# Kernel optimization log

Measured on AMD Instinct MI355X. Metric: run time of the kernel, lower is better.

The kernel has to match this reference:

```python
import jax, jax.numpy as jnp
import numpy as np

B, N, FEAT, HID, HEADS = 16, 1024, 512, 1024, 2

def setup_inputs() -> dict:
    key = jax.random.key(0)
    ks = jax.random.split(key, 20)
    s = 0.03
    d = {
        'Fs':  jax.random.normal(ks[0], (B, N, FEAT), jnp.float32),
        'Fq':  jax.random.normal(ks[1], (B, N, FEAT), jnp.float32),
        'Fms': jax.random.normal(ks[2], (B, N, FEAT), jnp.float32),
        'out_dim': N,
        'W1': jax.random.normal(ks[3], (FEAT, FEAT), jnp.float32) * s,
        'W2': jax.random.normal(ks[4], (FEAT, FEAT), jnp.float32) * s,
        'W3': jax.random.normal(ks[5], (FEAT, FEAT), jnp.float32) * s,
        'W4': jax.random.normal(ks[6], (FEAT, FEAT), jnp.float32) * s,
        'W5': jax.random.normal(ks[7], (FEAT, FEAT), jnp.float32) * s,
        'W6': jax.random.normal(ks[8], (FEAT, FEAT), jnp.float32) * s,
        'Wq': jax.random.normal(ks[9], (N, N), jnp.float32) * s,
        'Wk': jax.random.normal(ks[10], (N, N), jnp.float32) * s,
        'Wv': jax.random.normal(ks[11], (N, N), jnp.float32) * s,
        'ln_g': jnp.ones((N,), jnp.float32),
        'ln_b': jnp.zeros((N,), jnp.float32),
        'ffn_w1': jax.random.normal(ks[12], (N, HID), jnp.float32) * s,
        'ffn_w2': jax.random.normal(ks[13], (HID, N), jnp.float32) * s,
        'ffn_ln_g': jnp.ones((N,), jnp.float32),
        'ffn_ln_b': jnp.zeros((N,), jnp.float32),
    }
    return d

def _layernorm(x, g, b, eps):
    mu = x.mean(-1, keepdims=True)
    var = x.var(-1, keepdims=True)
    return (x - mu) * jax.lax.rsqrt(var + eps) * g + b

def _affinity(a, b, Wa, Wb, cl):
    # softmax((a Wa)(b Wb)^T / sqrt(cl)) over last axis
    s = jnp.einsum('bnc,bmc->bnm', a @ Wa, b @ Wb) / jnp.sqrt(jnp.float32(cl))
    return jax.nn.softmax(s, axis=-1)

def reference(Fs, Fq, Fms, out_dim, W1, W2, W3, W4, W5, W6, Wq, Wk, Wv,
              ln_g, ln_b, ffn_w1, ffn_w2, ffn_ln_g, ffn_ln_b):
    ass = _affinity(Fms, Fms, W1, W2, Fms.shape[2])   # [B,N,N]
    asq = _affinity(Fs, Fq, W3, W4, Fs.shape[2])      # [B,N,N]
    aqq = _affinity(Fq, Fq, W5, W6, Fq.shape[2])      # [B,N,N]

    Q, K, V = asq @ Wq, ass @ Wk, asq @ Wv            # [B,N,C], C=N
    Bb, Nn, C = Q.shape
    g = C // HEADS
    def heads(x):
        return x.reshape(Bb, Nn, HEADS, g).transpose(0, 2, 1, 3)  # [B,h,N,g]
    Qs, Ks, Vs = heads(Q), heads(K), heads(V)
    attn = jax.nn.softmax(jnp.einsum('bhqg,bhkg->bhqk', Qs, Ks) / jnp.sqrt(jnp.float32(g)), axis=-1)
    o = jnp.einsum('bhqk,bhkg->bhqg', attn, Vs)
    o = o.transpose(0, 2, 1, 3).reshape(Bb, Nn, C)

    x = _layernorm(o + aqq, ln_g, ln_b, 1e-5)
    y = jnp.maximum(x @ ffn_w1, 0.0) @ ffn_w2 + x     # dropout = identity (eval)
    y = _layernorm(y, ffn_ln_g, ffn_ln_b, 1e-6)
    return y
```

## Files before the change

kernel.cpp:

```cpp
#include <hip/hip_runtime.h>
#include <cstdint>

static constexpr long long Bb = 16, Nn = 1024, FE = 512;
static constexpr long long BN = Bb * Nn;
static constexpr long long E1e = BN * FE;
static constexpr long long E2n = BN * Nn;

static constexpr long long O_WT  = 0;
static constexpr long long SZ_W512 = FE * FE * 2;
static constexpr long long O_WQT = O_WT + 6 * SZ_W512;
static constexpr long long SZ_W1K = Nn * Nn * 2;
static constexpr long long O_WKT = O_WQT + SZ_W1K;
static constexpr long long O_WVT = O_WKT + SZ_W1K;
static constexpr long long O_F1T = O_WVT + SZ_W1K;
static constexpr long long O_F2T = O_F1T + SZ_W1K;
static constexpr long long O_SLOTS = O_F2T + SZ_W1K;
static constexpr long long SLOT = E2n * 2;
static constexpr long long O_S0 = O_SLOTS;
static constexpr long long O_S1 = O_S0 + SLOT;
static constexpr long long O_S2 = O_S1 + SLOT;
static constexpr long long O_E0 = O_S2 + SLOT;
static constexpr long long O_E1 = O_E0 + SLOT;
static constexpr long long O_E2 = O_E1 + SLOT;
static constexpr long long WS_NEED = O_E2 + SLOT;
static constexpr long long O_FMSB = O_E1;
static constexpr long long O_FSB  = O_E1 + E1e * 2;
static constexpr long long O_FQB  = O_E2;
static constexpr long long O_C2   = O_E2 + E1e * 2;

typedef __attribute__((ext_vector_type(8))) short short8;
typedef __attribute__((ext_vector_type(4))) float f32x4;

static __device__ __forceinline__ unsigned short f2bf(float f) {
  union { float f; unsigned u; } x; x.f = f;
  unsigned r = x.u + 0x7FFFu + ((x.u >> 16) & 1u);
  return (unsigned short)(r >> 16);
}
static __device__ __forceinline__ float bf2f(unsigned short h) {
  union { unsigned u; float f; } x; x.u = ((unsigned)h) << 16; return x.f;
}
static __device__ __forceinline__ void gload16(const void* g, void* l) {
  __builtin_amdgcn_global_load_lds(
      (const __attribute__((address_space(1))) unsigned int*)g,
      (__attribute__((address_space(3))) unsigned int*)l, 16, 0, 0);
}

template <int EP>
__global__ __launch_bounds__(256) void gemm_nt(
    const unsigned short* __restrict__ A, long long sA, long long hA, int lda,
    const unsigned short* __restrict__ B, long long sB, long long hB, int ldb,
    void* __restrict__ Cv, long long sC, long long hC, int ldc,
    const void* __restrict__ Rv, long long sR, int K) {
  __shared__ unsigned short lA[128 * 64];
  __shared__ unsigned short lB[64 * 64];
  const int tid = threadIdx.x;
  const int wave = tid >> 6, lane = tid & 63;
  const int wm = wave >> 1, wn = wave & 1;
  const int lrow = lane & 15, quad = lane >> 4;
  const int z = blockIdx.z, z1 = z & 15, z2 = z >> 4;
  const int gy = gridDim.y;
  const int bid = blockIdx.x + gridDim.x * blockIdx.y;
  const int chunk = 8 * gy;
  const int bx = (bid / chunk) * 8 + (bid % 8);
  const int by = (bid % chunk) / 8;
  const long long bm = (long long)bx * 128;
  const long long bn = (long long)by * 64;
  const unsigned short* Ab = A + z1 * sA + z2 * hA + bm * lda;
  const unsigned short* Bbp = B + z1 * sB + z2 * hB + bn * ldb;
  const int srow = lane >> 2;
  const int skol = (lane & 3) * 8;
  const int g0 = wave * 2, g1 = wave * 2 + 1;

  f32x4 acc[4][2];
#pragma unroll
  for (int i = 0; i < 4; ++i)
#pragma unroll
    for (int j = 0; j < 2; ++j) acc[i][j] = (f32x4){0.f, 0.f, 0.f, 0.f};

  for (int k0 = 0; k0 < K; k0 += 64) {
    const unsigned short* Ak = Ab + k0 + skol;
    const unsigned short* Bk = Bbp + k0 + skol;
    gload16(Ak + (long long)(g0 * 16 + srow) * lda,      &lA[g0 * 512 + lane * 8]);
    gload16(Ak + (long long)(g1 * 16 + srow) * lda,      &lA[g1 * 512 + lane * 8]);
    gload16(Ak + (long long)(g0 * 16 + srow) * lda + 32, &lA[4096 + g0 * 512 + lane * 8]);
    gload16(Ak + (long long)(g1 * 16 + srow) * lda + 32, &lA[4096 + g1 * 512 + lane * 8]);
    gload16(Bk + (long long)(wave * 16 + srow) * ldb,      &lB[wave * 512 + lane * 8]);
    gload16(Bk + (long long)(wave * 16 + srow) * ldb + 32, &lB[2048 + wave * 512 + lane * 8]);
    __syncthreads();
#pragma unroll
    for (int p = 0; p < 2; ++p) {
      short8 af[4], bfr[2];
#pragma unroll
      for (int t = 0; t < 4; ++t)
        af[t] = *(const short8*)&lA[p * 4096 + (wm * 64 + t * 16 + lrow) * 32 + quad * 8];
#pragma unroll
      for (int u = 0; u < 2; ++u)
        bfr[u] = *(const short8*)&lB[p * 2048 + (wn * 32 + u * 16 + lrow) * 32 + quad * 8];
#pragma unroll
      for (int mt = 0; mt < 4; ++mt)
#pragma unroll
        for (int nt = 0; nt < 2; ++nt)
          acc[mt][nt] = __builtin_amdgcn_mfma_f32_16x16x32_bf16(af[mt], bfr[nt], acc[mt][nt], 0, 0, 0);
    }
    __syncthreads();
  }
  const long long cm = bm + wm * 64, cn = bn + wn * 32;
  const long long cz = z1 * sC + z2 * hC;
#pragma unroll
  for (int mt = 0; mt < 4; ++mt) {
#pragma unroll
    for (int nt = 0; nt < 2; ++nt) {
      long long col = cn + nt * 16 + lrow;
      long long row0 = cm + mt * 16 + quad * 4;
#pragma unroll
      for (int r = 0; r < 4; ++r) {
        long long row = row0 + r;
        float v = acc[mt][nt][r];
        long long idx = cz + row * ldc + col;
        if (EP == 1) ((unsigned short*)Cv)[idx] = f2bf(v);
        else if (EP == 2) ((unsigned short*)Cv)[idx] = f2bf(v > 0.f ? v : 0.f);
        else {
          float rr = bf2f(((const unsigned short*)Rv)[z1 * sR + row * ldc + col]);
          ((float*)Cv)[idx] = v + rr;
        }
      }
    }
  }
}

__global__ __launch_bounds__(256) void cast3_k(const float* __restrict__ i0,
                                               const float* __restrict__ i1,
                                               const float* __restrict__ i2,
                                               unsigned short* o0, unsigned short* o1,
                                               unsigned short* o2) {
  const float* in = (blockIdx.y == 0) ? i0 : (blockIdx.y == 1) ? i1 : i2;
  unsigned short* out = (blockIdx.y == 0) ? o0 : (blockIdx.y == 1) ? o1 : o2;
  long long i = (long long)blockIdx.x * 256 + threadIdx.x;
  float4 v = ((const float4*)in)[i];
  ushort4 o; o.x = f2bf(v.x); o.y = f2bf(v.y); o.z = f2bf(v.z); o.w = f2bf(v.w);
  ((ushort4*)out)[i] = o;
}

__global__ __launch_bounds__(256) void tcast6_k(const float* p0, const float* p1,
                                                const float* p2, const float* p3,
                                                const float* p4, const float* p5,
                                                unsigned short* outb, int rows, int cols) {
  const float* src[6] = {p0, p1, p2, p3, p4, p5};
  const float* in = src[blockIdx.z];
  unsigned short* out = outb + (long long)blockIdx.z * rows * cols;
  __shared__ float t[32][33];
  const int c0 = blockIdx.x * 32, r0 = blockIdx.y * 32;
  const int tx = threadIdx.x, ty = threadIdx.y;
#pragma unroll
  for (int i = 0; i < 4; ++i) {
    int r = r0 + ty + i * 8;
    t[ty + i * 8][tx] = in[(long long)r * cols + c0 + tx];
  }
  __syncthreads();
#pragma unroll
  for (int i = 0; i < 4; ++i) {
    int c = c0 + ty + i * 8;
    out[(long long)c * rows + r0 + tx] = f2bf(t[tx][ty + i * 8]);
  }
}

__global__ __launch_bounds__(256) void softmax_bf(unsigned short* __restrict__ S, float scale) {
  __shared__ float redA[4], redB[4];
  const long long row = blockIdx.x;
  const int t = threadIdx.x, wave = t >> 6, lane = t & 63;
  ushort4 u = ((ushort4*)(S + row * 1024))[t];
  float v0 = bf2f(u.x) * scale, v1 = bf2f(u.y) * scale, v2 = bf2f(u.z) * scale, v3 = bf2f(u.w) * scale;
  float m = fmaxf(fmaxf(v0, v1), fmaxf(v2, v3));
#pragma unroll
  for (int o = 32; o; o >>= 1) m = fmaxf(m, __shfl_down(m, o));
  if (lane == 0) redA[wave] = m;
  __syncthreads();
  m = fmaxf(fmaxf(redA[0], redA[1]), fmaxf(redA[2], redA[3]));
  float e0 = __expf(v0 - m), e1 = __expf(v1 - m), e2 = __expf(v2 - m), e3 = __expf(v3 - m);
  float s = e0 + e1 + e2 + e3;
#pragma unroll
  for (int o = 32; o; o >>= 1) s += __shfl_down(s, o);
  if (lane == 0) redB[wave] = s;
  __syncthreads();
  s = redB[0] + redB[1] + redB[2] + redB[3];
  float inv = 1.f / s;
  ushort4 ob; ob.x = f2bf(e0 * inv); ob.y = f2bf(e1 * inv); ob.z = f2bf(e2 * inv); ob.w = f2bf(e3 * inv);
  ((ushort4*)(S + row * 1024))[t] = ob;
}

__global__ __launch_bounds__(256) void ln1_k(const unsigned short* __restrict__ O,
                                             const unsigned short* __restrict__ Aq,
                                             const float* __restrict__ g, const float* __restrict__ b,
                                             unsigned short* __restrict__ xb) {
  __shared__ float redA[4], redB[4];
  const long long row = blockIdx.x;
  const int t = threadIdx.x, wave = t >> 6, lane = t & 63;
  ushort4 ou = ((const ushort4*)(O + row * 1024))[t];
  ushort4 au = ((const ushort4*)(Aq + row * 1024))[t];
  float v0 = bf2f(ou.x) + bf2f(au.x), v1 = bf2f(ou.y) + bf2f(au.y);
  float v2 = bf2f(ou.z) + bf2f(au.z), v3 = bf2f(ou.w) + bf2f(au.w);
  float s = v0 + v1 + v2 + v3;
  float q = v0 * v0 + v1 * v1 + v2 * v2 + v3 * v3;
#pragma unroll
  for (int o = 32; o; o >>= 1) { s += __shfl_down(s, o); q += __shfl_down(q, o); }
  if (lane == 0) { redA[wave] = s; redB[wave] = q; }
  __syncthreads();
  float S = redA[0] + redA[1] + redA[2] + redA[3];
  float Q = redB[0] + redB[1] + redB[2] + redB[3];
  float mu = S * (1.f / 1024.f);
  float var = Q * (1.f / 1024.f) - mu * mu;
  float rs = rsqrtf(var + 1e-5f);
  float4 gg = ((const float4*)g)[t], bbv = ((const float4*)b)[t];
  ushort4 ob;
  ob.x = f2bf((v0 - mu) * rs * gg.x + bbv.x);
  ob.y = f2bf((v1 - mu) * rs * gg.y + bbv.y);
  ob.z = f2bf((v2 - mu) * rs * gg.z + bbv.z);
  ob.w = f2bf((v3 - mu) * rs * gg.w + bbv.w);
  ((ushort4*)(xb + row * 1024))[t] = ob;
}

__global__ __launch_bounds__(256) void ln2_k(const float* __restrict__ Y,
                                             const float* __restrict__ g, const float* __restrict__ b,
                                             float* __restrict__ out, float eps) {
  __shared__ float redA[4], redB[4];
  const long long row = blockIdx.x;
  const int t = threadIdx.x, wave = t >> 6, lane = t & 63;
  float4 v = ((const float4*)(Y + row * 1024))[t];
  float s = v.x + v.y + v.z + v.w;
  float q = v.x * v.x + v.y * v.y + v.z * v.z + v.w * v.w;
#pragma unroll
  for (int o = 32; o; o >>= 1) { s += __shfl_down(s, o); q += __shfl_down(q, o); }
  if (lane == 0) { redA[wave] = s; redB[wave] = q; }
  __syncthreads();
  float S = redA[0] + redA[1] + redA[2] + redA[3];
  float Q = redB[0] + redB[1] + redB[2] + redB[3];
  float mu = S * (1.f / 1024.f);
  float var = Q * (1.f / 1024.f) - mu * mu;
  float rs = rsqrtf(var + eps);
  float4 gg = ((const float4*)g)[t], bbv = ((const float4*)b)[t];
  float4 o;
  o.x = (v.x - mu) * rs * gg.x + bbv.x;
  o.y = (v.y - mu) * rs * gg.y + bbv.y;
  o.z = (v.z - mu) * rs * gg.z + bbv.z;
  o.w = (v.w - mu) * rs * gg.w + bbv.w;
  ((float4*)(out + row * 1024))[t] = o;
}

extern "C" void kernel_launch(void* const* d_in, const int* in_sizes, int n_in,
                              void* d_out, int out_size, void* d_ws, size_t ws_size,
                              hipStream_t stream) {
  (void)in_sizes; (void)n_in; (void)out_size;
  if (ws_size < (size_t)WS_NEED) return;

  const float* Fs  = (const float*)d_in[0];
  const float* Fq  = (const float*)d_in[1];
  const float* Fms = (const float*)d_in[2];
  const float* Wm[6] = {(const float*)d_in[4], (const float*)d_in[5], (const float*)d_in[6],
                        (const float*)d_in[7], (const float*)d_in[8], (const float*)d_in[9]};
  const float* Wq = (const float*)d_in[10];
  const float* Wk = (const float*)d_in[11];
  const float* Wv = (const float*)d_in[12];
  const float* ln_g = (const float*)d_in[13];
  const float* ln_b = (const float*)d_in[14];
  const float* fw1 = (const float*)d_in[15];
  const float* fw2 = (const float*)d_in[16];
  const float* fg = (const float*)d_in[17];
  const float* fb = (const float*)d_in[18];
  float* out = (float*)d_out;
  uint8_t* ws = (uint8_t*)d_ws;
  auto U16 = [&](long long off) { return (unsigned short*)(ws + off); };

  const float inv_sqrt512 = 0.04419417382415922f;
  dim3 blk(256);

  auto gemm = [&](int ep, const unsigned short* A, long long sA, long long hA, int lda,
                  const unsigned short* B, long long sB, long long hB, int ldb,
                  void* C, long long sC, long long hC, int ldc, const void* R, long long sR,
                  int M, int N, int K, int batch) {
    dim3 g(M / 128, N / 64, batch);
    switch (ep) {
      case 1: gemm_nt<1><<<g, blk, 0, stream>>>(A, sA, hA, lda, B, sB, hB, ldb, C, sC, hC, ldc, R, sR, K); break;
      case 2: gemm_nt<2><<<g, blk, 0, stream>>>(A, sA, hA, lda, B, sB, hB, ldb, C, sC, hC, ldc, R, sR, K); break;
      default: gemm_nt<3><<<g, blk, 0, stream>>>(A, sA, hA, lda, B, sB, hB, ldb, C, sC, hC, ldc, R, sR, K); break;
    }
  };

  tcast6_k<<<dim3(16, 16, 6), dim3(32, 8), 0, stream>>>(
      Wm[0], Wm[1], Wm[2], Wm[3], Wm[4], Wm[5], U16(O_WT), 512, 512);
  tcast6_k<<<dim3(32, 32, 5), dim3(32, 8), 0, stream>>>(
      Wq, Wk, Wv, fw1, fw2, fw2 , U16(O_WQT), 1024, 1024);
  cast3_k<<<dim3(E1e / 4 / 256, 3), blk, 0, stream>>>(
      Fs, Fq, Fms, U16(O_FSB), U16(O_FQB), U16(O_FMSB));

  gemm(1, U16(O_FMSB), 0, 0, 512, U16(O_WT), 0, 0, 512, U16(O_S0), 0, 0, 1024,
       nullptr, 0, (int)BN, 1024, 512, 1);
  gemm(1, U16(O_S0), Nn * 1024, 0, 1024, U16(O_S0) + 512, Nn * 1024, 0, 1024,
       U16(O_E0), Nn * Nn, 0, 1024, nullptr, 0, 1024, 1024, 512, (int)Bb);
  softmax_bf<<<dim3(BN), blk, 0, stream>>>(U16(O_E0), inv_sqrt512);

  gemm(1, U16(O_FSB), 0, 0, 512, U16(O_WT + 2 * SZ_W512), 0, 0, 512, U16(O_C2), 0, 0, 512,
       nullptr, 0, (int)BN, 512, 512, 1);
  gemm(1, U16(O_FQB), 0, 0, 512, U16(O_WT + 3 * SZ_W512), 0, 0, 512, U16(O_S1), 0, 0, 1024,
       nullptr, 0, (int)BN, 1024, 512, 1);
  gemm(1, U16(O_FQB), 0, 0, 512, U16(O_WT + 5 * SZ_W512), 0, 0, 512, U16(O_S2), 0, 0, 512,
       nullptr, 0, (int)BN, 512, 512, 1);
  gemm(1, U16(O_C2), Nn * 512, 0, 512, U16(O_S1), Nn * 1024, 0, 1024,
       U16(O_E1), Nn * Nn, 0, 1024, nullptr, 0, 1024, 1024, 512, (int)Bb);
  softmax_bf<<<dim3(BN), blk, 0, stream>>>(U16(O_E1), inv_sqrt512);
  gemm(1, U16(O_S1) + 512, Nn * 1024, 0, 1024, U16(O_S2), Nn * 512, 0, 512,
       U16(O_E2), Nn * Nn, 0, 1024, nullptr, 0, 1024, 1024, 512, (int)Bb);
  softmax_bf<<<dim3(BN), blk, 0, stream>>>(U16(O_E2), inv_sqrt512);

  const unsigned short* assB = U16(O_E0);
  const unsigned short* asqB = U16(O_E1);

  gemm(1, assB, Nn * Nn, E2n, 1024,
       U16(O_WKT), 0, -(long long)(SZ_W1K / 2), 1024,
       U16(O_S1), Nn * 1024, -(long long)E2n, 1024,
       nullptr, 0, 1024, 1024, 1024, 32);
  gemm(1, U16(O_WVT), 0, 0, 1024, asqB, Nn * Nn, 0, 1024, U16(O_S2), Nn * Nn, 0, 1024,
       nullptr, 0, 1024, 1024, 1024, (int)Bb);

  gemm(1, U16(O_S0), Nn * 1024, 512, 1024, U16(O_S1), Nn * 1024, 512, 1024,
       U16(O_E0), Nn * Nn, 16 * Nn * Nn, 1024, nullptr, 0, 1024, 1024, 512, 32);
  softmax_bf<<<dim3(2 * BN), blk, 0, stream>>>(U16(O_E0), inv_sqrt512);

  gemm(1, U16(O_E0), Nn * Nn, 16 * Nn * Nn, 1024, U16(O_S2), Nn * Nn, 512 * 1024, 1024,
       U16(O_S0), Nn * 1024, 512, 1024, nullptr, 0, 1024, 512, 1024, 32);

  ln1_k<<<dim3(BN), blk, 0, stream>>>(U16(O_S0), U16(O_E2), ln_g, ln_b, U16(O_S1));

  gemm(2, U16(O_S1), 0, 0, 1024, U16(O_F1T), 0, 0, 1024, U16(O_S2), 0, 0, 1024,
       nullptr, 0, (int)BN, 1024, 1024, 1);

  gemm(3, U16(O_S2), 0, 0, 1024, U16(O_F2T), 0, 0, 1024, out, 0, 0, 1024,
       U16(O_S1), 0, (int)BN, 1024, 1024, 1);

  ln2_k<<<dim3(BN), blk, 0, stream>>>(out, fg, fb, out, 1e-6f);
}
```

Measured before the change: 856.1 us.

## Replace GEMM with 256x256-tile pipelined kernel and merge projection/softmax launches

Replaces the 128x64 GEMM with a 512-thread 256x256 tile kernel. It uses a 4-stage LDS ring buffer (128KB dynamic LDS) filled by direct global-to-LDS loads, an XOR swizzle against bank conflicts, s_setprio around the MFMA block, and an XCD-aware workgroup remap. It also merges several projection GEMMs into batched launches through stride tricks (including a negative output stride) and fuses the three softmax launches into one. The goal is more data reuse per tile, better load/compute overlap and fewer launches. The risks are fewer workgroups for small problems and fragile stride arithmetic.

```diff
diff --git a/kernel.cpp b/kernel.cpp
--- a/kernel.cpp
+++ b/kernel.cpp
@@ -46,76 +46,105 @@
 }
 
 template <int EP>
-__global__ __launch_bounds__(256) void gemm_nt(
+__global__ __launch_bounds__(512, 2) void gemm256(
     const unsigned short* __restrict__ A, long long sA, long long hA, int lda,
     const unsigned short* __restrict__ B, long long sB, long long hB, int ldb,
     void* __restrict__ Cv, long long sC, long long hC, int ldc,
     const void* __restrict__ Rv, long long sR, int K) {
-  __shared__ unsigned short lA[128 * 64];
-  __shared__ unsigned short lB[64 * 64];
+  extern __shared__ unsigned short lds[];
   const int tid = threadIdx.x;
-  const int wave = tid >> 6, lane = tid & 63;
-  const int wm = wave >> 1, wn = wave & 1;
+  const int lane = tid & 63;
+  const int wave = tid >> 6;
+  const int wm = wave >> 2, wn = wave & 3;
   const int lrow = lane & 15, quad = lane >> 4;
-  const int z = blockIdx.z, z1 = z & 15, z2 = z >> 4;
-  const int gy = gridDim.y;
-  const int bid = blockIdx.x + gridDim.x * blockIdx.y;
-  const int chunk = 8 * gy;
-  const int bx = (bid / chunk) * 8 + (bid % 8);
-  const int by = (bid % chunk) / 8;
-  const long long bm = (long long)bx * 128;
-  const long long bn = (long long)by * 64;
+
+  const int gx = gridDim.x;
+  const int nxy = gx * gridDim.y;
+  const int nwg = nxy * gridDim.z;
+  int wg = blockIdx.x + gx * blockIdx.y + nxy * blockIdx.z;
+  wg = (wg & 7) * (nwg >> 3) + (wg >> 3);
+  const int bz = wg / nxy;
+  const int rem = wg - bz * nxy;
+  const int by = rem / gx;
+  const int bx = rem - by * gx;
+  const int z1 = bz & 15, z2 = bz >> 4;
+
+  const long long bm = (long long)bx * 256;
+  const long long bn = (long long)by * 256;
   const unsigned short* Ab = A + z1 * sA + z2 * hA + bm * lda;
-  const unsigned short* Bbp = B + z1 * sB + z2 * hB + bn * ldb;
-  const int srow = lane >> 2;
-  const int skol = (lane & 3) * 8;
-  const int g0 = wave * 2, g1 = wave * 2 + 1;
-
-  f32x4 acc[4][2];
-#pragma unroll
-  for (int i = 0; i < 4; ++i)
-#pragma unroll
-    for (int j = 0; j < 2; ++j) acc[i][j] = (f32x4){0.f, 0.f, 0.f, 0.f};
-
-  for (int k0 = 0; k0 < K; k0 += 64) {
-    const unsigned short* Ak = Ab + k0 + skol;
-    const unsigned short* Bk = Bbp + k0 + skol;
-    gload16(Ak + (long long)(g0 * 16 + srow) * lda,      &lA[g0 * 512 + lane * 8]);
-    gload16(Ak + (long long)(g1 * 16 + srow) * lda,      &lA[g1 * 512 + lane * 8]);
-    gload16(Ak + (long long)(g0 * 16 + srow) * lda + 32, &lA[4096 + g0 * 512 + lane * 8]);
-    gload16(Ak + (long long)(g1 * 16 + srow) * lda + 32, &lA[4096 + g1 * 512 + lane * 8]);
-    gload16(Bk + (long long)(wave * 16 + srow) * ldb,      &lB[wave * 512 + lane * 8]);
-    gload16(Bk + (long long)(wave * 16 + srow) * ldb + 32, &lB[2048 + wave * 512 + lane * 8]);
-    __syncthreads();
-#pragma unroll
-    for (int p = 0; p < 2; ++p) {
-      short8 af[4], bfr[2];
-#pragma unroll
-      for (int t = 0; t < 4; ++t)
-        af[t] = *(const short8*)&lA[p * 4096 + (wm * 64 + t * 16 + lrow) * 32 + quad * 8];
-#pragma unroll
-      for (int u = 0; u < 2; ++u)
-        bfr[u] = *(const short8*)&lB[p * 2048 + (wn * 32 + u * 16 + lrow) * 32 + quad * 8];
-#pragma unroll
-      for (int mt = 0; mt < 4; ++mt)
-#pragma unroll
-        for (int nt = 0; nt < 2; ++nt)
-          acc[mt][nt] = __builtin_amdgcn_mfma_f32_16x16x32_bf16(af[mt], bfr[nt], acc[mt][nt], 0, 0, 0);
-    }
-    __syncthreads();
+  const unsigned short* Bp = B + z1 * sB + z2 * hB + bn * ldb;
+
+  const int srow = tid >> 2;
+  const int scol = ((tid & 3) ^ ((tid >> 3) & 3)) * 8;
+  unsigned short* ldst = lds + tid * 8;
+
+  auto STAGE = [&](int tt) {
+    unsigned short* d = ldst + (tt & 3) * 16384;
+    const long long ko = (long long)tt * 32 + scol;
+    gload16(Ab + (long long)srow * lda + ko, d);
+    gload16(Ab + (long long)(srow + 128) * lda + ko, d + 4096);
+    gload16(Bp + (long long)srow * ldb + ko, d + 8192);
+    gload16(Bp + (long long)(srow + 128) * ldb + ko, d + 12288);
+  };
+
+  const int swq = (quad ^ ((lrow >> 1) & 3)) * 8;
+  const int a_off = (wm * 128 + lrow) * 32 + swq;
+  const int b_off = 8192 + (wn * 64 + lrow) * 32 + swq;
+
+  f32x4 acc[8][4];
+#pragma unroll
+  for (int m = 0; m < 8; ++m)
+#pragma unroll
+    for (int n = 0; n < 4; ++n) acc[m][n] = (f32x4){0.f, 0.f, 0.f, 0.f};
+
+  auto COMPUTE = [&](int tt) {
+    const unsigned short* lb = lds + (tt & 3) * 16384;
+    short8 af[8], bfr[4];
+#pragma unroll
+    for (int m = 0; m < 8; ++m) af[m] = *(const short8*)&lb[a_off + m * 512];
+#pragma unroll
+    for (int n = 0; n < 4; ++n) bfr[n] = *(const short8*)&lb[b_off + n * 512];
+    __builtin_amdgcn_s_setprio(1);
+#pragma unroll
+    for (int m = 0; m < 8; ++m)
+#pragma unroll
+      for (int n = 0; n < 4; ++n)
+        acc[m][n] = __builtin_amdgcn_mfma_f32_16x16x32_bf16(af[m], bfr[n], acc[m][n], 0, 0, 0);
+    __builtin_amdgcn_s_setprio(0);
+  };
+
+  const int nt = K >> 5;
+  STAGE(0); STAGE(1); STAGE(2);
+  int t = 0;
+  for (; t < nt - 3; ++t) {
+    STAGE(t + 3);
+    asm volatile("s_waitcnt vmcnt(12)" ::: "memory");
+    __builtin_amdgcn_s_barrier();
+    COMPUTE(t);
+    __builtin_amdgcn_s_barrier();
   }
-  const long long cm = bm + wm * 64, cn = bn + wn * 32;
+  asm volatile("s_waitcnt vmcnt(8)" ::: "memory");
+  __builtin_amdgcn_s_barrier();
+  COMPUTE(t); ++t;
+  asm volatile("s_waitcnt vmcnt(4)" ::: "memory");
+  __builtin_amdgcn_s_barrier();
+  COMPUTE(t); ++t;
+  asm volatile("s_waitcnt vmcnt(0)" ::: "memory");
+  __builtin_amdgcn_s_barrier();
+  COMPUTE(t);
+
+  const long long cm = bm + wm * 128, cn = bn + wn * 64;
   const long long cz = z1 * sC + z2 * hC;
 #pragma unroll
-  for (int mt = 0; mt < 4; ++mt) {
-#pragma unroll
-    for (int nt = 0; nt < 2; ++nt) {
-      long long col = cn + nt * 16 + lrow;
+  for (int mt = 0; mt < 8; ++mt) {
+#pragma unroll
+    for (int ntl = 0; ntl < 4; ++ntl) {
+      long long col = cn + ntl * 16 + lrow;
       long long row0 = cm + mt * 16 + quad * 4;
 #pragma unroll
       for (int r = 0; r < 4; ++r) {
         long long row = row0 + r;
-        float v = acc[mt][nt][r];
+        float v = acc[mt][ntl][r];
         long long idx = cz + row * ldc + col;
         if (EP == 1) ((unsigned short*)Cv)[idx] = f2bf(v);
         else if (EP == 2) ((unsigned short*)Cv)[idx] = f2bf(v > 0.f ? v : 0.f);
@@ -251,6 +280,17 @@
                               hipStream_t stream) {
   (void)in_sizes; (void)n_in; (void)out_size;
   if (ws_size < (size_t)WS_NEED) return;
+
+  static int attr_once = []() {
+    (void)hipFuncSetAttribute(reinterpret_cast<const void*>(&gemm256<1>),
+                              hipFuncAttributeMaxDynamicSharedMemorySize, 131072);
+    (void)hipFuncSetAttribute(reinterpret_cast<const void*>(&gemm256<2>),
+                              hipFuncAttributeMaxDynamicSharedMemorySize, 131072);
+    (void)hipFuncSetAttribute(reinterpret_cast<const void*>(&gemm256<3>),
+                              hipFuncAttributeMaxDynamicSharedMemorySize, 131072);
+    return 0;
+  }();
+  (void)attr_once;
 
   const float* Fs  = (const float*)d_in[0];
   const float* Fq  = (const float*)d_in[1];
@@ -277,11 +317,12 @@
                   const unsigned short* B, long long sB, long long hB, int ldb,
                   void* C, long long sC, long long hC, int ldc, const void* R, long long sR,
                   int M, int N, int K, int batch) {
-    dim3 g(M / 128, N / 64, batch);
+    dim3 g(M / 256, N / 256, batch);
+    dim3 b(512);
     switch (ep) {
-      case 1: gemm_nt<1><<<g, blk, 0, stream>>>(A, sA, hA, lda, B, sB, hB, ldb, C, sC, hC, ldc, R, sR, K); break;
-      case 2: gemm_nt<2><<<g, blk, 0, stream>>>(A, sA, hA, lda, B, sB, hB, ldb, C, sC, hC, ldc, R, sR, K); break;
-      default: gemm_nt<3><<<g, blk, 0, stream>>>(A, sA, hA, lda, B, sB, hB, ldb, C, sC, hC, ldc, R, sR, K); break;
+      case 1: gemm256<1><<<g, b, 131072, stream>>>(A, sA, hA, lda, B, sB, hB, ldb, C, sC, hC, ldc, R, sR, K); break;
+      case 2: gemm256<2><<<g, b, 131072, stream>>>(A, sA, hA, lda, B, sB, hB, ldb, C, sC, hC, ldc, R, sR, K); break;
+      default: gemm256<3><<<g, b, 131072, stream>>>(A, sA, hA, lda, B, sB, hB, ldb, C, sC, hC, ldc, R, sR, K); break;
     }
   };
 
@@ -292,33 +333,25 @@
   cast3_k<<<dim3(E1e / 4 / 256, 3), blk, 0, stream>>>(
       Fs, Fq, Fms, U16(O_FSB), U16(O_FQB), U16(O_FMSB));
 
-  gemm(1, U16(O_FMSB), 0, 0, 512, U16(O_WT), 0, 0, 512, U16(O_S0), 0, 0, 1024,
-       nullptr, 0, (int)BN, 1024, 512, 1);
+  gemm(1, U16(O_FMSB), 16777216, 0, 512, U16(O_WT), 786432, 0, 512,
+       U16(O_S0), 16777216, 0, 1024, nullptr, 0, (int)BN, 1024, 512, 2);
   gemm(1, U16(O_S0), Nn * 1024, 0, 1024, U16(O_S0) + 512, Nn * 1024, 0, 1024,
        U16(O_E0), Nn * Nn, 0, 1024, nullptr, 0, 1024, 1024, 512, (int)Bb);
-  softmax_bf<<<dim3(BN), blk, 0, stream>>>(U16(O_E0), inv_sqrt512);
-
-  gemm(1, U16(O_FSB), 0, 0, 512, U16(O_WT + 2 * SZ_W512), 0, 0, 512, U16(O_C2), 0, 0, 512,
-       nullptr, 0, (int)BN, 512, 512, 1);
-  gemm(1, U16(O_FQB), 0, 0, 512, U16(O_WT + 3 * SZ_W512), 0, 0, 512, U16(O_S1), 0, 0, 1024,
-       nullptr, 0, (int)BN, 1024, 512, 1);
-  gemm(1, U16(O_FQB), 0, 0, 512, U16(O_WT + 5 * SZ_W512), 0, 0, 512, U16(O_S2), 0, 0, 512,
-       nullptr, 0, (int)BN, 512, 512, 1);
+  gemm(1, U16(O_FSB), 8388608, 0, 512, U16(O_WT + 2 * SZ_W512), 786432, 0, 512,
+       U16(O_C2), -58720256LL, 0, 512, nullptr, 0, (int)BN, 512, 512, 2);
   gemm(1, U16(O_C2), Nn * 512, 0, 512, U16(O_S1), Nn * 1024, 0, 1024,
        U16(O_E1), Nn * Nn, 0, 1024, nullptr, 0, 1024, 1024, 512, (int)Bb);
-  softmax_bf<<<dim3(BN), blk, 0, stream>>>(U16(O_E1), inv_sqrt512);
   gemm(1, U16(O_S1) + 512, Nn * 1024, 0, 1024, U16(O_S2), Nn * 512, 0, 512,
        U16(O_E2), Nn * Nn, 0, 1024, nullptr, 0, 1024, 1024, 512, (int)Bb);
-  softmax_bf<<<dim3(BN), blk, 0, stream>>>(U16(O_E2), inv_sqrt512);
+  softmax_bf<<<dim3(3 * BN), blk, 0, stream>>>(U16(O_E0), inv_sqrt512);
 
   const unsigned short* assB = U16(O_E0);
-  const unsigned short* asqB = U16(O_E1);
 
   gemm(1, assB, Nn * Nn, E2n, 1024,
        U16(O_WKT), 0, -(long long)(SZ_W1K / 2), 1024,
        U16(O_S1), Nn * 1024, -(long long)E2n, 1024,
        nullptr, 0, 1024, 1024, 1024, 32);
-  gemm(1, U16(O_WVT), 0, 0, 1024, asqB, Nn * Nn, 0, 1024, U16(O_S2), Nn * Nn, 0, 1024,
+  gemm(1, U16(O_WVT), 0, 0, 1024, U16(O_E1), Nn * Nn, 0, 1024, U16(O_S2), Nn * Nn, 0, 1024,
        nullptr, 0, 1024, 1024, 1024, (int)Bb);
 
   gemm(1, U16(O_S0), Nn * 1024, 512, 1024, U16(O_S1), Nn * 1024, 512, 1024,
```

New measurement: 723.4 us. -15.5%, faster.
